# Performance work log

Hardware: AMD Instinct MI355X
Metric: run time of the kernel (lower is better)

## Reference

```python
import jax, jax.numpy as jnp
import numpy as np

B, S, E = 8, 2048, 1024
DROPOUT_P = 0.1


def setup_inputs() -> dict:
    key = jax.random.key(0)
    kq, kk, kv, km, kw, kb = jax.random.split(key, 6)
    query = jax.random.normal(kq, (B, S, E), dtype=jnp.float32)
    key_t = jax.random.normal(kk, (B, S, E), dtype=jnp.float32)
    value = jax.random.normal(kv, (B, S, E), dtype=jnp.float32)
    # inverted dropout mask: keep with prob 1-p, scale kept by 1/(1-p)
    keep = jax.random.bernoulli(km, 1.0 - DROPOUT_P, (B, S, S))
    dropout_mask = keep.astype(jnp.float32) / (1.0 - DROPOUT_P)
    Wout = jax.random.normal(kw, (E, E), dtype=jnp.float32) * (E ** -0.5)
    bout = jax.random.normal(kb, (E,), dtype=jnp.float32) * 0.01
    return {
        "query": query,
        "key": key_t,
        "value": value,
        "dropout_mask": dropout_mask,
        "Wout": Wout,
        "bout": bout,
        "inv_scale_factor": 32,  # sqrt(E) = sqrt(1024)
    }


def reference(query, key, value, dropout_mask, Wout, bout, inv_scale_factor):
    # scores: [B, S, S]
    scores = jnp.einsum("bqd,bkd->bqk", query, key) / jnp.float32(inv_scale_factor)
    probs = jax.nn.softmax(scores, axis=-1)
    probs = probs * dropout_mask  # inverted dropout
    attn = jnp.einsum("bqk,bkd->bqd", probs, value)  # [B, S, E]
    # fc_out: torch Linear -> x @ W.T + b
    return jnp.einsum("bqd,ed->bqe", attn, Wout) + bout
```

## Files before the change

### kernel.cpp

```cpp
#include <hip/hip_runtime.h>
#include <cstdint>
#include <cstddef>

typedef short short8 __attribute__((ext_vector_type(8)));
typedef float f32x4 __attribute__((ext_vector_type(4)));

static __device__ __forceinline__ ushort f2bf(float f) {
  union { float f; uint32_t u; } v; v.f = f;
  uint32_t u = v.u + 0x7fffu + ((v.u >> 16) & 1u);
  return (ushort)(u >> 16);
}
static __device__ __forceinline__ float b2f(uint32_t u) {
  union { uint32_t u; float f; } v; v.u = u << 16;
  return v.f;
}

__global__ __launch_bounds__(256) void transpose_convert_v(
    const float* __restrict__ V, ushort* __restrict__ Vt) {
  __shared__ float t[32][33];
  const int b = blockIdx.z;
  const int d0 = blockIdx.x * 32;
  const int k0 = blockIdx.y * 32;
  const int tx = threadIdx.x, ty = threadIdx.y;
  const float* Vb = V + (size_t)b * 2048 * 1024;
  ushort* Vtb = Vt + (size_t)b * 1024 * 2048;
#pragma unroll
  for (int j = 0; j < 32; j += 8)
    t[ty + j][tx] = Vb[(size_t)(k0 + ty + j) * 1024 + d0 + tx];
  __syncthreads();
#pragma unroll
  for (int j = 0; j < 32; j += 8)
    Vtb[(size_t)(d0 + ty + j) * 2048 + k0 + tx] = f2bf(t[tx][ty + j]);
}

template <bool A_F32, bool B_F32, bool OUT_BF16, bool BIAS>
__global__ __launch_bounds__(256) void gemm_bt(
    const void* __restrict__ Ap, const void* __restrict__ Bp,
    void* __restrict__ Cp, int M, int N, int K,
    size_t sA, size_t sB, size_t sC, float scale,
    const float* __restrict__ bias) {
  constexpr int BK = 64, LDT = 72;
  __shared__ __align__(16) ushort As[128 * LDT];
  __shared__ __align__(16) ushort Bs[128 * LDT];
  const int tid = threadIdx.x;
  const int z = blockIdx.z;
  const int bm = blockIdx.y, bn = blockIdx.x;
  const int lane = tid & 63, w = tid >> 6;
  const int quad = lane >> 4, l16 = lane & 15;
  const int row0 = (w & 1) * 64, col0 = (w >> 1) * 64;

  f32x4 acc[4][4];
#pragma unroll
  for (int i = 0; i < 4; ++i)
#pragma unroll
    for (int j = 0; j < 4; ++j) acc[i][j] = (f32x4){0.f, 0.f, 0.f, 0.f};

  for (int k0 = 0; k0 < K; k0 += BK) {
    if constexpr (A_F32) {
      const float* A = (const float*)Ap + sA * z + (size_t)bm * 128 * K + k0;
      int r = tid >> 4;
      const int c = (tid & 15) * 4;
#pragma unroll
      for (int i = 0; i < 8; ++i, r += 16) {
        const float4 v = *(const float4*)(A + (size_t)r * K + c);
        ushort4 o;
        o.x = f2bf(v.x); o.y = f2bf(v.y); o.z = f2bf(v.z); o.w = f2bf(v.w);
        *(ushort4*)&As[r * LDT + c] = o;
      }
    } else {
      const ushort* A = (const ushort*)Ap + sA * z + (size_t)bm * 128 * K + k0;
      int r = tid >> 3;
      const int c = (tid & 7) * 8;
#pragma unroll
      for (int i = 0; i < 4; ++i, r += 32)
        *(uint4*)&As[r * LDT + c] = *(const uint4*)(A + (size_t)r * K + c);
    }
    if constexpr (B_F32) {
      const float* B = (const float*)Bp + sB * z + (size_t)bn * 128 * K + k0;
      int r = tid >> 4;
      const int c = (tid & 15) * 4;
#pragma unroll
      for (int i = 0; i < 8; ++i, r += 16) {
        const float4 v = *(const float4*)(B + (size_t)r * K + c);
        ushort4 o;
        o.x = f2bf(v.x); o.y = f2bf(v.y); o.z = f2bf(v.z); o.w = f2bf(v.w);
        *(ushort4*)&Bs[r * LDT + c] = o;
      }
    } else {
      const ushort* B = (const ushort*)Bp + sB * z + (size_t)bn * 128 * K + k0;
      int r = tid >> 3;
      const int c = (tid & 7) * 8;
#pragma unroll
      for (int i = 0; i < 4; ++i, r += 32)
        *(uint4*)&Bs[r * LDT + c] = *(const uint4*)(B + (size_t)r * K + c);
    }
    __syncthreads();
#pragma unroll
    for (int kc = 0; kc < BK; kc += 32) {
      short8 af[4], bfr[4];
#pragma unroll
      for (int tm = 0; tm < 4; ++tm)
        af[tm] = *(const short8*)&As[(row0 + tm * 16 + l16) * LDT + kc + quad * 8];
#pragma unroll
      for (int tn = 0; tn < 4; ++tn)
        bfr[tn] = *(const short8*)&Bs[(col0 + tn * 16 + l16) * LDT + kc + quad * 8];
#pragma unroll
      for (int tm = 0; tm < 4; ++tm)
#pragma unroll
        for (int tn = 0; tn < 4; ++tn)
          acc[tm][tn] = __builtin_amdgcn_mfma_f32_16x16x32_bf16(
              af[tm], bfr[tn], acc[tm][tn], 0, 0, 0);
    }
    __syncthreads();
  }
#pragma unroll
  for (int tn = 0; tn < 4; ++tn) {
    const int gc = bn * 128 + col0 + tn * 16 + l16;
    const float bv = BIAS ? bias[gc] : 0.f;
#pragma unroll
    for (int tm = 0; tm < 4; ++tm) {
      const int grb = bm * 128 + row0 + tm * 16 + quad * 4;
#pragma unroll
      for (int r = 0; r < 4; ++r) {
        const float v = acc[tm][tn][r] * scale + bv;
        const size_t idx = (size_t)(grb + r) * N + gc;
        if constexpr (OUT_BF16)
          ((ushort*)Cp + sC * z)[idx] = f2bf(v);
        else
          ((float*)Cp + sC * z)[idx] = v;
      }
    }
  }
}

__global__ __launch_bounds__(256) void softmax_dropout(
    ushort* __restrict__ P, const float* __restrict__ mask) {
  const int row = blockIdx.x;
  const size_t off = (size_t)row * 2048 + (size_t)threadIdx.x * 8;
  ushort* p = P + off;
  const float* mk = mask + off;
  const uint4 raw = *(const uint4*)p;
  float s[8];
  s[0] = b2f(raw.x & 0xffffu); s[1] = b2f(raw.x >> 16);
  s[2] = b2f(raw.y & 0xffffu); s[3] = b2f(raw.y >> 16);
  s[4] = b2f(raw.z & 0xffffu); s[5] = b2f(raw.z >> 16);
  s[6] = b2f(raw.w & 0xffffu); s[7] = b2f(raw.w >> 16);
  float m = s[0];
#pragma unroll
  for (int i = 1; i < 8; ++i) m = fmaxf(m, s[i]);
#pragma unroll
  for (int o = 32; o >= 1; o >>= 1) m = fmaxf(m, __shfl_xor(m, o));
  __shared__ float redm[4], reds[4];
  const int wv = threadIdx.x >> 6;
  if ((threadIdx.x & 63) == 0) redm[wv] = m;
  __syncthreads();
  m = fmaxf(fmaxf(redm[0], redm[1]), fmaxf(redm[2], redm[3]));
  float e[8], l = 0.f;
#pragma unroll
  for (int i = 0; i < 8; ++i) { e[i] = __expf(s[i] - m); l += e[i]; }
#pragma unroll
  for (int o = 32; o >= 1; o >>= 1) l += __shfl_xor(l, o);
  if ((threadIdx.x & 63) == 0) reds[wv] = l;
  __syncthreads();
  l = (reds[0] + reds[1]) + (reds[2] + reds[3]);
  const float inv = 1.0f / l;
  const float4 m0 = *(const float4*)mk;
  const float4 m1 = *(const float4*)(mk + 4);
  float q[8];
  q[0] = e[0] * inv * m0.x; q[1] = e[1] * inv * m0.y;
  q[2] = e[2] * inv * m0.z; q[3] = e[3] * inv * m0.w;
  q[4] = e[4] * inv * m1.x; q[5] = e[5] * inv * m1.y;
  q[6] = e[6] * inv * m1.z; q[7] = e[7] * inv * m1.w;
  uint4 o;
  o.x = (uint32_t)f2bf(q[0]) | ((uint32_t)f2bf(q[1]) << 16);
  o.y = (uint32_t)f2bf(q[2]) | ((uint32_t)f2bf(q[3]) << 16);
  o.z = (uint32_t)f2bf(q[4]) | ((uint32_t)f2bf(q[5]) << 16);
  o.w = (uint32_t)f2bf(q[6]) | ((uint32_t)f2bf(q[7]) << 16);
  *(uint4*)p = o;
}

extern "C" void kernel_launch(void* const* d_in, const int* in_sizes, int n_in,
                              void* d_out, int out_size, void* d_ws,
                              size_t ws_size, hipStream_t stream) {
  (void)in_sizes; (void)n_in; (void)out_size; (void)ws_size;
  const float* Q    = (const float*)d_in[0];
  const float* Kmat = (const float*)d_in[1];
  const float* V    = (const float*)d_in[2];
  const float* mask = (const float*)d_in[3];
  const float* W    = (const float*)d_in[4];
  const float* bout = (const float*)d_in[5];
  float* out = (float*)d_out;

  ushort* Vt   = (ushort*)d_ws;
  ushort* P    = Vt + (size_t)8 * 1024 * 2048;
  ushort* attn = P + (size_t)8 * 2048 * 2048;

  transpose_convert_v<<<dim3(32, 64, 8), dim3(32, 8), 0, stream>>>(V, Vt);
  gemm_bt<true, true, true, false><<<dim3(16, 16, 8), 256, 0, stream>>>(
      Q, Kmat, P, 2048, 2048, 1024,
      (size_t)2048 * 1024, (size_t)2048 * 1024, (size_t)2048 * 2048,
      1.0f / 32.0f, nullptr);
  softmax_dropout<<<dim3(16384), 256, 0, stream>>>(P, mask);
  gemm_bt<false, false, true, false><<<dim3(8, 16, 8), 256, 0, stream>>>(
      P, Vt, attn, 2048, 1024, 2048,
      (size_t)2048 * 2048, (size_t)1024 * 2048, (size_t)2048 * 1024,
      1.0f, nullptr);
  gemm_bt<false, true, false, true><<<dim3(8, 128, 1), 256, 0, stream>>>(
      attn, W, out, 16384, 1024, 1024, 0, 0, 0, 1.0f, bout);
}
```

Baseline: 659.1 us.

## Pre-convert Q/K to bf16 and load GEMM tiles directly into LDS

Q and K are now converted to bf16 once in a separate elementwise kernel, so the score GEMM reads half the bytes and skips repeated in-loop conversion. All bf16 operand tiles are loaded with global_load_lds, which writes straight to shared memory without passing through registers. To fit that path the LDS tiles drop their row padding to a 64-element stride, and the workspace buffers are reused. The unpadded layout risks bank conflicts on the 16-byte fragment reads, and the conversion passes add extra launches and memory traffic.

```diff
diff --git a/kernel.cpp b/kernel.cpp
--- a/kernel.cpp
+++ b/kernel.cpp
@@ -13,6 +13,25 @@
 static __device__ __forceinline__ float b2f(uint32_t u) {
   union { uint32_t u; float f; } v; v.u = u << 16;
   return v.f;
+}
+
+static __device__ __forceinline__ void g2lds16(const ushort* g, ushort* lds) {
+  __builtin_amdgcn_global_load_lds(
+      (const __attribute__((address_space(1))) void*)(uintptr_t)g,
+      (__attribute__((address_space(3))) void*)(uintptr_t)lds,
+      16, 0, 0);
+}
+
+__global__ __launch_bounds__(256) void convert_f32_bf16(
+    const float* __restrict__ src, ushort* __restrict__ dst) {
+  const size_t i = ((size_t)blockIdx.x * 256 + threadIdx.x) * 8;
+  const float4 a = *(const float4*)(src + i);
+  const float4 b = *(const float4*)(src + i + 4);
+  ushort4 o0, o1;
+  o0.x = f2bf(a.x); o0.y = f2bf(a.y); o0.z = f2bf(a.z); o0.w = f2bf(a.w);
+  o1.x = f2bf(b.x); o1.y = f2bf(b.y); o1.z = f2bf(b.z); o1.w = f2bf(b.w);
+  *(ushort4*)(dst + i) = o0;
+  *(ushort4*)(dst + i + 4) = o1;
 }
 
 __global__ __launch_bounds__(256) void transpose_convert_v(
@@ -33,21 +52,24 @@
     Vtb[(size_t)(d0 + ty + j) * 2048 + k0 + tx] = f2bf(t[tx][ty + j]);
 }
 
-template <bool A_F32, bool B_F32, bool OUT_BF16, bool BIAS>
+template <bool B_F32, bool OUT_BF16, bool BIAS>
 __global__ __launch_bounds__(256) void gemm_bt(
-    const void* __restrict__ Ap, const void* __restrict__ Bp,
+    const ushort* __restrict__ Ap, const void* __restrict__ Bp,
     void* __restrict__ Cp, int M, int N, int K,
     size_t sA, size_t sB, size_t sC, float scale,
     const float* __restrict__ bias) {
-  constexpr int BK = 64, LDT = 72;
-  __shared__ __align__(16) ushort As[128 * LDT];
-  __shared__ __align__(16) ushort Bs[128 * LDT];
+  constexpr int BK = 64;
+  constexpr int LDB = B_F32 ? 72 : 64;
+  __shared__ __align__(16) ushort As[128 * 64];
+  __shared__ __align__(16) ushort Bs[128 * LDB];
   const int tid = threadIdx.x;
   const int z = blockIdx.z;
   const int bm = blockIdx.y, bn = blockIdx.x;
   const int lane = tid & 63, w = tid >> 6;
   const int quad = lane >> 4, l16 = lane & 15;
   const int row0 = (w & 1) * 64, col0 = (w >> 1) * 64;
+  const int srow = lane >> 3;
+  const int scol = (lane & 7) * 8;
 
   f32x4 acc[4][4];
 #pragma unroll
@@ -55,25 +77,13 @@
 #pragma unroll
     for (int j = 0; j < 4; ++j) acc[i][j] = (f32x4){0.f, 0.f, 0.f, 0.f};
 
+  const ushort* Abase = Ap + sA * z + (size_t)bm * 128 * K;
+
   for (int k0 = 0; k0 < K; k0 += BK) {
-    if constexpr (A_F32) {
-      const float* A = (const float*)Ap + sA * z + (size_t)bm * 128 * K + k0;
-      int r = tid >> 4;
-      const int c = (tid & 15) * 4;
-#pragma unroll
-      for (int i = 0; i < 8; ++i, r += 16) {
-        const float4 v = *(const float4*)(A + (size_t)r * K + c);
-        ushort4 o;
-        o.x = f2bf(v.x); o.y = f2bf(v.y); o.z = f2bf(v.z); o.w = f2bf(v.w);
-        *(ushort4*)&As[r * LDT + c] = o;
-      }
-    } else {
-      const ushort* A = (const ushort*)Ap + sA * z + (size_t)bm * 128 * K + k0;
-      int r = tid >> 3;
-      const int c = (tid & 7) * 8;
-#pragma unroll
-      for (int i = 0; i < 4; ++i, r += 32)
-        *(uint4*)&As[r * LDT + c] = *(const uint4*)(A + (size_t)r * K + c);
+#pragma unroll
+    for (int i = 0; i < 4; ++i) {
+      const int rbase = w * 8 + i * 32;
+      g2lds16(Abase + (size_t)(rbase + srow) * K + k0 + scol, &As[rbase * 64]);
     }
     if constexpr (B_F32) {
       const float* B = (const float*)Bp + sB * z + (size_t)bn * 128 * K + k0;
@@ -84,15 +94,15 @@
         const float4 v = *(const float4*)(B + (size_t)r * K + c);
         ushort4 o;
         o.x = f2bf(v.x); o.y = f2bf(v.y); o.z = f2bf(v.z); o.w = f2bf(v.w);
-        *(ushort4*)&Bs[r * LDT + c] = o;
+        *(ushort4*)&Bs[r * LDB + c] = o;
       }
     } else {
       const ushort* B = (const ushort*)Bp + sB * z + (size_t)bn * 128 * K + k0;
-      int r = tid >> 3;
-      const int c = (tid & 7) * 8;
-#pragma unroll
-      for (int i = 0; i < 4; ++i, r += 32)
-        *(uint4*)&Bs[r * LDT + c] = *(const uint4*)(B + (size_t)r * K + c);
+#pragma unroll
+      for (int i = 0; i < 4; ++i) {
+        const int rbase = w * 8 + i * 32;
+        g2lds16(B + (size_t)(rbase + srow) * K + scol, &Bs[rbase * 64]);
+      }
     }
     __syncthreads();
 #pragma unroll
@@ -100,10 +110,10 @@
       short8 af[4], bfr[4];
 #pragma unroll
       for (int tm = 0; tm < 4; ++tm)
-        af[tm] = *(const short8*)&As[(row0 + tm * 16 + l16) * LDT + kc + quad * 8];
+        af[tm] = *(const short8*)&As[(row0 + tm * 16 + l16) * 64 + kc + quad * 8];
 #pragma unroll
       for (int tn = 0; tn < 4; ++tn)
-        bfr[tn] = *(const short8*)&Bs[(col0 + tn * 16 + l16) * LDT + kc + quad * 8];
+        bfr[tn] = *(const short8*)&Bs[(col0 + tn * 16 + l16) * LDB + kc + quad * 8];
 #pragma unroll
       for (int tm = 0; tm < 4; ++tm)
 #pragma unroll
@@ -191,20 +201,22 @@
   const float* bout = (const float*)d_in[5];
   float* out = (float*)d_out;
 
-  ushort* Vt   = (ushort*)d_ws;
-  ushort* P    = Vt + (size_t)8 * 1024 * 2048;
-  ushort* attn = P + (size_t)8 * 2048 * 2048;
-
-  transpose_convert_v<<<dim3(32, 64, 8), dim3(32, 8), 0, stream>>>(V, Vt);
-  gemm_bt<true, true, true, false><<<dim3(16, 16, 8), 256, 0, stream>>>(
-      Q, Kmat, P, 2048, 2048, 1024,
+  ushort* RegA = (ushort*)d_ws;
+  ushort* RegB = RegA + (size_t)16 * 1024 * 1024;
+  ushort* P    = RegB + (size_t)16 * 1024 * 1024;
+
+  convert_f32_bf16<<<dim3(8192), 256, 0, stream>>>(Q, RegA);
+  convert_f32_bf16<<<dim3(8192), 256, 0, stream>>>(Kmat, RegB);
+  gemm_bt<false, true, false><<<dim3(16, 16, 8), 256, 0, stream>>>(
+      RegA, RegB, P, 2048, 2048, 1024,
       (size_t)2048 * 1024, (size_t)2048 * 1024, (size_t)2048 * 2048,
       1.0f / 32.0f, nullptr);
+  transpose_convert_v<<<dim3(32, 64, 8), dim3(32, 8), 0, stream>>>(V, RegA);
   softmax_dropout<<<dim3(16384), 256, 0, stream>>>(P, mask);
-  gemm_bt<false, false, true, false><<<dim3(8, 16, 8), 256, 0, stream>>>(
-      P, Vt, attn, 2048, 1024, 2048,
+  gemm_bt<false, true, false><<<dim3(8, 16, 8), 256, 0, stream>>>(
+      P, RegA, RegB, 2048, 1024, 2048,
       (size_t)2048 * 2048, (size_t)1024 * 2048, (size_t)2048 * 1024,
       1.0f, nullptr);
-  gemm_bt<false, true, false, true><<<dim3(8, 128, 1), 256, 0, stream>>>(
-      attn, W, out, 16384, 1024, 1024, 0, 0, 0, 1.0f, bout);
-}
+  gemm_bt<true, false, true><<<dim3(8, 128, 1), 256, 0, stream>>>(
+      RegB, W, out, 16384, 1024, 1024, 0, 0, 0, 1.0f, bout);
+}
```

New measurement: 625.7 us. 5.1% less time.
